# Kernel tuning notes

Hardware: AMD Instinct MI355X
Metric: run time of the kernel (lower is better)

The kernel has to match this reference:

```python
import jax, jax.numpy as jnp
import numpy as np

B, N, E, DIN, DH = 32, 2000, 64000, 128, 128


def setup_inputs() -> dict:
    key = jax.random.key(0)
    ks = jax.random.split(key, 8)
    gene_emb = jax.random.normal(ks[0], (B, N, DIN), dtype=jnp.float32)
    edge_src = jax.random.randint(ks[1], (E,), 0, N, dtype=jnp.int32)
    edge_dst = jax.random.randint(ks[2], (E,), 0, N, dtype=jnp.int32)
    s1 = 1.0 / np.sqrt(DIN)
    s2 = 1.0 / np.sqrt(DH)
    W1 = jax.random.normal(ks[3], (DIN, DH), dtype=jnp.float32) * s1
    b1 = jnp.zeros((DH,), dtype=jnp.float32)
    W2 = jax.random.normal(ks[4], (DH, DH), dtype=jnp.float32) * s2
    b2 = jnp.zeros((DH,), dtype=jnp.float32)
    return {"gene_emb": gene_emb, "edge_src": edge_src, "edge_dst": edge_dst,
            "W1": W1, "b1": b1, "W2": W2, "b2": b2, "pathway_idx": 0}


def _gcn_conv(x, src, dst, norm_e, self_norm, W, b):
    # x: [B, N, Din] -> [B, N, Dout]; PyG GCNConv: linear first, then normalized aggregation
    h = jnp.einsum('bnd,de->bne', x, W)
    msgs = h[:, src, :] * norm_e[None, :, None]          # [B, E, Dout] gather
    agg = jax.vmap(lambda m: jax.ops.segment_sum(m, dst, num_segments=h.shape[1]))(msgs)
    # self-loop contribution (A+I): norm = dinv[i]^2
    return agg + h * self_norm[None, :, None] + b


def reference(gene_emb, edge_src, edge_dst, W1, b1, W2, b2, pathway_idx):
    n = gene_emb.shape[1]
    # symmetric GCN normalization with self loops: deg[i] = in_degree + 1
    deg = jnp.zeros((n,), dtype=gene_emb.dtype).at[edge_dst].add(1.0) + 1.0
    dinv = jax.lax.rsqrt(deg)
    norm_e = dinv[edge_src] * dinv[edge_dst]
    self_norm = dinv * dinv
    x = jax.nn.relu(_gcn_conv(gene_emb, edge_src, edge_dst, norm_e, self_norm, W1, b1))
    x = _gcn_conv(x, edge_src, edge_dst, norm_e, self_norm, W2, b2)
    # global_mean_pool over each graph copy (all graphs have n nodes)
    return jnp.mean(x, axis=1)  # [B, DH]
```

## Files before the change

kernel.cpp:

```cpp
#include <hip/hip_runtime.h>

namespace {
constexpr int NB = 32;
constexpr int NN = 2000;
constexpr int NE = 64000;
constexpr int ND = 128;
constexpr int TR = 32;
constexpr int NCHUNK = (NN + TR - 1) / TR;
constexpr int NXCD = 8;
constexpr int BPB = 2;
constexpr int PAIRS = NB / (NXCD * BPB);
constexpr int GRID_FUSED = NXCD * PAIRS * NCHUNK;
constexpr int SL = 80;
constexpr int ECAP = 1536;

constexpr int CVT_BLOCKS  = 8000;
constexpr int NODE_BLOCKS = 250;
constexpr int W_BLOCKS    = 8;
constexpr int PREP_GRID   = CVT_BLOCKS + NODE_BLOCKS + W_BLOCKS;

constexpr size_t OFF_CNT  = 0;
constexpr size_t OFF_OCNT = 8192;
constexpr size_t OFF_SLI  = 16384;
constexpr size_t OFF_SLO  = OFF_SLI + (size_t)NN * SL * 4;
constexpr size_t OFF_WF   = OFF_SLO + (size_t)NN * SL * 4;
constexpr size_t OFF_XBF  = OFF_WF + 32768;
constexpr size_t OFF_YP   = OFF_XBF + (size_t)NB * NN * ND * 2;

typedef __attribute__((ext_vector_type(8))) short bf16x8;
typedef __attribute__((ext_vector_type(4))) float f32x4;

__device__ __forceinline__ ushort f32_to_bf16(float f) {
    uint u = __float_as_uint(f);
    u += 0x7fffu + ((u >> 16) & 1u);
    return (ushort)(u >> 16);
}
__device__ __forceinline__ uint pack_bf16x2(float lo, float hi) {
    return (uint)f32_to_bf16(lo) | ((uint)f32_to_bf16(hi) << 16);
}
}

__global__ void k_prep(const float* __restrict__ X, ushort* __restrict__ xbf,
                       const float* __restrict__ W1, uint* __restrict__ wf,
                       const int* __restrict__ src, const int* __restrict__ dst,
                       int* __restrict__ cnt, int* __restrict__ ocnt,
                       int* __restrict__ slot_in, int* __restrict__ slot_out) {
    const int blk = blockIdx.x;
    const int tid = threadIdx.x;
    if (blk < CVT_BLOCKS) {
        int i = blk * 256 + tid;
        float4 v = ((const float4*)X)[i];
        ushort4 o;
        o.x = f32_to_bf16(v.x);
        o.y = f32_to_bf16(v.y);
        o.z = f32_to_bf16(v.z);
        o.w = f32_to_bf16(v.w);
        ((ushort4*)xbf)[i] = o;
    } else if (blk < CVT_BLOCKS + NODE_BLOCKS) {
        const int base = (blk - CVT_BLOCKS) * 8;
        __shared__ int lcin[8], lcout[8];
        if (tid < 8) { lcin[tid] = 0; lcout[tid] = 0; }
        __syncthreads();
        const int4* s4p = (const int4*)src;
        const int4* d4p = (const int4*)dst;
        for (int i = tid; i < NE / 4; i += 256) {
            int4 s4 = s4p[i], d4 = d4p[i];
            int ss[4] = {s4.x, s4.y, s4.z, s4.w};
            int dd[4] = {d4.x, d4.y, d4.z, d4.w};
            #pragma unroll
            for (int q = 0; q < 4; q++) {
                int j = dd[q] - base;
                if ((unsigned)j < 8u) {
                    int p = atomicAdd(&lcin[j], 1);
                    if (p < SL) slot_in[(size_t)dd[q] * SL + p] = ss[q];
                }
                int j2 = ss[q] - base;
                if ((unsigned)j2 < 8u) {
                    int p2 = atomicAdd(&lcout[j2], 1);
                    if (p2 < SL) slot_out[(size_t)ss[q] * SL + p2] = dd[q];
                }
            }
        }
        __syncthreads();
        if (tid < 8) {
            cnt[base + tid]  = lcin[tid];
            ocnt[base + tid] = lcout[tid];
        }
    } else {
        int g = (blk - CVT_BLOCKS - NODE_BLOCKS) * 256 + tid;
        int lane = g & 63, f = g >> 6;
        int nt = f >> 2, kc = f & 3;
        int col = nt * 16 + (lane & 15);
        int k0  = kc * 32 + (lane >> 4) * 8;
        uint4 o;
        o.x = pack_bf16x2(W1[(k0 + 0) * ND + col], W1[(k0 + 1) * ND + col]);
        o.y = pack_bf16x2(W1[(k0 + 2) * ND + col], W1[(k0 + 3) * ND + col]);
        o.z = pack_bf16x2(W1[(k0 + 4) * ND + col], W1[(k0 + 5) * ND + col]);
        o.w = pack_bf16x2(W1[(k0 + 6) * ND + col], W1[(k0 + 7) * ND + col]);
        ((uint4*)wf)[g] = o;
    }
}

__global__ __launch_bounds__(256, 4) void k_fused(const ushort* __restrict__ xbf,
                                                  const int* __restrict__ cnt,
                                                  const int* __restrict__ ocnt,
                                                  const int* __restrict__ slot_in,
                                                  const int* __restrict__ slot_out,
                                                  const uint* __restrict__ wfrag,
                                                  const float* __restrict__ b1,
                                                  float* __restrict__ ypart) {
    __shared__ uint  AsU[2][32 * 68];
    __shared__ int2  sEdge[ECAP];
    __shared__ int   sCnt[32];
    __shared__ int   sBase[33];
    __shared__ float sDinv[32];
    __shared__ float sWn[32];
    __shared__ float yred[2][128];
    const int tid = threadIdx.x;

    const int L     = blockIdx.x;
    const int xcd   = L & (NXCD - 1);
    const int sl    = L >> 3;
    const int pair  = sl / NCHUNK;
    const int chunk = sl % NCHUNK;
    const int b0    = xcd * (BPB * PAIRS) + pair * BPB;
    const int n0    = chunk * TR;

    if (tid < 32) {
        int n = n0 + tid;
        int cr = (n < NN) ? cnt[n] : 0;
        sCnt[tid]  = min(cr, SL);
        sDinv[tid] = rsqrtf((float)(cr + 1));
    }
    if (tid < 128) { yred[0][tid] = 0.f; yred[1][tid] = 0.f; }
    __syncthreads();
    if (tid == 0) {
        int s = 0;
        for (int j = 0; j < 32; j++) { sBase[j] = s; s += sCnt[j]; }
        sBase[32] = s;
    }

    const int wv = tid >> 6, ln = tid & 63;

    for (int ii = 0; ii < 8; ii++) {
        const int j = wv * 8 + ii;
        const int n = n0 + j;
        float part = 0.f;
        if (n < NN) {
            int oc = min(ocnt[n], SL);
            const int* op = &slot_out[(size_t)n * SL];
            for (int base = 0; base < oc; base += 64)
                if (base + ln < oc)
                    part += rsqrtf((float)(cnt[op[base + ln]] + 1));
        }
        #pragma unroll
        for (int off = 32; off; off >>= 1) part += __shfl_down(part, off, 64);
        if (ln == 0) {
            float d = sDinv[j];
            sWn[j] = (n < NN) ? d * (d + part) : 0.f;
        }
    }
    __syncthreads();
    const bool staged = (sBase[32] <= ECAP);

    if (staged) {
        for (int ii = 0; ii < 8; ii++) {
            int j = wv * 8 + ii;
            int c = sCnt[j];
            float dd = sDinv[j];
            const int* sp = &slot_in[(size_t)(n0 + j) * SL];
            for (int base = 0; base < c; base += 64) {
                if (base + ln < c) {
                    int sidx = sp[base + ln];
                    float w = rsqrtf((float)(cnt[sidx] + 1)) * dd;
                    sEdge[sBase[j] + base + ln] = make_int2(sidx, __float_as_int(w));
                }
            }
        }
    }
    __syncthreads();

    const uint* __restrict__ Xu0 = (const uint*)(xbf + (size_t)b0 * NN * ND);
    const uint* __restrict__ Xu1 = (const uint*)(xbf + (size_t)(b0 + 1) * NN * ND);
    #pragma unroll 1
    for (int ii = 0; ii < 8; ii++) {
        const int j = wv * 8 + ii;
        const int n = n0 + j;
        float2 a0 = make_float2(0.f, 0.f), a1 = a0, a0b = a0, a1b = a0;
        if (n < NN) {
            float sn = sDinv[j]; sn *= sn;
            uint u0 = Xu0[n * 64 + ln], u1 = Xu1[n * 64 + ln];
            a0.x = sn * __uint_as_float(u0 << 16);
            a0.y = sn * __uint_as_float(u0 & 0xffff0000u);
            a1.x = sn * __uint_as_float(u1 << 16);
            a1.y = sn * __uint_as_float(u1 & 0xffff0000u);
            const int c = sCnt[j];
            if (staged) {
                const int e0 = sBase[j], e1 = e0 + c;
                int e = e0;
                for (; e + 8 <= e1; e += 8) {
                    int sidx[8]; float w[8]; uint q0[8], q1[8];
                    #pragma unroll
                    for (int q = 0; q < 8; q++) {
                        int2 ed = sEdge[e + q];
                        sidx[q] = ed.x; w[q] = __int_as_float(ed.y);
                    }
                    #pragma unroll
                    for (int q = 0; q < 8; q++) {
                        q0[q] = Xu0[sidx[q] * 64 + ln];
                        q1[q] = Xu1[sidx[q] * 64 + ln];
                    }
                    #pragma unroll
                    for (int q = 0; q < 8; q++) {
                        float x0l = __uint_as_float(q0[q] << 16);
                        float x0h = __uint_as_float(q0[q] & 0xffff0000u);
                        float x1l = __uint_as_float(q1[q] << 16);
                        float x1h = __uint_as_float(q1[q] & 0xffff0000u);
                        if (q & 1) {
                            a0b.x = fmaf(w[q], x0l, a0b.x);
                            a0b.y = fmaf(w[q], x0h, a0b.y);
                            a1b.x = fmaf(w[q], x1l, a1b.x);
                            a1b.y = fmaf(w[q], x1h, a1b.y);
                        } else {
                            a0.x = fmaf(w[q], x0l, a0.x);
                            a0.y = fmaf(w[q], x0h, a0.y);
                            a1.x = fmaf(w[q], x1l, a1.x);
                            a1.y = fmaf(w[q], x1h, a1.y);
                        }
                    }
                }
                for (; e < e1; e++) {
                    int2 ed = sEdge[e];
                    float w = __int_as_float(ed.y);
                    uint u0e = Xu0[ed.x * 64 + ln], u1e = Xu1[ed.x * 64 + ln];
                    a0.x = fmaf(w, __uint_as_float(u0e << 16), a0.x);
                    a0.y = fmaf(w, __uint_as_float(u0e & 0xffff0000u), a0.y);
                    a1.x = fmaf(w, __uint_as_float(u1e << 16), a1.x);
                    a1.y = fmaf(w, __uint_as_float(u1e & 0xffff0000u), a1.y);
                }
            } else {
                const int* sp = &slot_in[(size_t)n * SL];
                float dd = sDinv[j];
                for (int e = 0; e < c; e++) {
                    int sidx = sp[e];
                    float w = rsqrtf((float)(cnt[sidx] + 1)) * dd;
                    uint u0e = Xu0[sidx * 64 + ln], u1e = Xu1[sidx * 64 + ln];
                    a0.x = fmaf(w, __uint_as_float(u0e << 16), a0.x);
                    a0.y = fmaf(w, __uint_as_float(u0e & 0xffff0000u), a0.y);
                    a1.x = fmaf(w, __uint_as_float(u1e << 16), a1.x);
                    a1.y = fmaf(w, __uint_as_float(u1e & 0xffff0000u), a1.y);
                }
            }
            a0.x += a0b.x; a0.y += a0b.y;
            a1.x += a1b.x; a1.y += a1b.y;
        }
        AsU[0][j * 68 + ln] = pack_bf16x2(a0.x, a0.y);
        AsU[1][j * 68 + ln] = pack_bf16x2(a1.x, a1.y);
    }
    __syncthreads();

    const int lane15 = ln & 15, quad = ln >> 4;
    f32x4 zero4 = {0.f, 0.f, 0.f, 0.f};
    f32x4 acc[2][2][2];
    #pragma unroll
    for (int b = 0; b < 2; b++)
        #pragma unroll
        for (int mt = 0; mt < 2; mt++)
            #pragma unroll
            for (int nt2 = 0; nt2 < 2; nt2++) acc[b][mt][nt2] = zero4;

    bf16x8 wfr[2][4];
    const bf16x8* Wf8 = (const bf16x8*)wfrag;
    #pragma unroll
    for (int nt2 = 0; nt2 < 2; nt2++)
        #pragma unroll
        for (int kc = 0; kc < 4; kc++)
            wfr[nt2][kc] = Wf8[(((2 * wv + nt2) * 4 + kc) * 64) + ln];

    const bf16x8* A8_0 = (const bf16x8*)AsU[0];
    const bf16x8* A8_1 = (const bf16x8*)AsU[1];
    #pragma unroll
    for (int mt = 0; mt < 2; mt++) {
        const int r = mt * 16 + lane15;
        #pragma unroll
        for (int kc = 0; kc < 4; kc++) {
            bf16x8 af0 = A8_0[r * 17 + kc * 4 + quad];
            bf16x8 af1 = A8_1[r * 17 + kc * 4 + quad];
            #pragma unroll
            for (int nt2 = 0; nt2 < 2; nt2++) {
                acc[0][mt][nt2] = __builtin_amdgcn_mfma_f32_16x16x32_bf16(
                    af0, wfr[nt2][kc], acc[0][mt][nt2], 0, 0, 0);
                acc[1][mt][nt2] = __builtin_amdgcn_mfma_f32_16x16x32_bf16(
                    af1, wfr[nt2][kc], acc[1][mt][nt2], 0, 0, 0);
            }
        }
    }

    #pragma unroll
    for (int nt2 = 0; nt2 < 2; nt2++) {
        int cg = (2 * wv + nt2) * 16 + lane15;
        float bias = b1[cg];
        #pragma unroll
        for (int b = 0; b < 2; b++) {
            float part = 0.f;
            #pragma unroll
            for (int mt = 0; mt < 2; mt++) {
                f32x4 a = acc[b][mt][nt2];
                #pragma unroll
                for (int r = 0; r < 4; r++) {
                    int m = mt * 16 + quad * 4 + r;
                    part = fmaf(sWn[m], fmaxf(a[r] + bias, 0.f), part);
                }
            }
            atomicAdd(&yred[b][cg], part);
        }
    }
    __syncthreads();
    if (tid < 128)
        ypart[((size_t)b0 * NCHUNK + chunk) * ND + tid] = yred[0][tid];
    else
        ypart[((size_t)(b0 + 1) * NCHUNK + chunk) * ND + (tid - 128)] = yred[1][tid - 128];
}

__global__ __launch_bounds__(128) void k_out(const float* __restrict__ ypart,
                                             const float* __restrict__ W2,
                                             const float* __restrict__ b2,
                                             float* __restrict__ out) {
    __shared__ float ys[128];
    const int b = blockIdx.x;
    const int d = threadIdx.x;
    float s = 0.f;
    for (int c = 0; c < NCHUNK; c++)
        s += ypart[((size_t)b * NCHUNK + c) * ND + d];
    ys[d] = s * (1.f / (float)NN);
    __syncthreads();
    float acc = b2[d];
    #pragma unroll 8
    for (int k = 0; k < 128; k++)
        acc = fmaf(ys[k], W2[k * ND + d], acc);
    out[b * ND + d] = acc;
}

extern "C" void kernel_launch(void* const* d_in, const int* in_sizes, int n_in,
                              void* d_out, int out_size, void* d_ws, size_t ws_size,
                              hipStream_t stream) {
    (void)in_sizes; (void)n_in; (void)out_size; (void)ws_size;
    const float* X   = (const float*)d_in[0];
    const int*   src = (const int*)d_in[1];
    const int*   dst = (const int*)d_in[2];
    const float* W1  = (const float*)d_in[3];
    const float* b1  = (const float*)d_in[4];
    const float* W2  = (const float*)d_in[5];
    const float* b2  = (const float*)d_in[6];
    float* out = (float*)d_out;

    char* ws = (char*)d_ws;
    int*    cnt   = (int*)   (ws + OFF_CNT);
    int*    ocnt  = (int*)   (ws + OFF_OCNT);
    int*    sli   = (int*)   (ws + OFF_SLI);
    int*    slo   = (int*)   (ws + OFF_SLO);
    uint*   wfb   = (uint*)  (ws + OFF_WF);
    ushort* xbf   = (ushort*)(ws + OFF_XBF);
    float*  ypart = (float*) (ws + OFF_YP);

    k_prep<<<PREP_GRID, 256, 0, stream>>>(X, xbf, W1, wfb, src, dst,
                                          cnt, ocnt, sli, slo);
    k_fused<<<GRID_FUSED, 256, 0, stream>>>(xbf, cnt, ocnt, sli, slo, wfb, b1, ypart);
    k_out<<<NB, 128, 0, stream>>>(ypart, W2, b2, out);
}
```

Measured before the change: 184.7 us.

## Build edge slot lists with global atomics and drop shared-memory edge staging

The per-node scan blocks, where each of 250 blocks reads all 64000 edges, are replaced by one thread per edge doing global atomicAdd into cnt/ocnt and slot lists, preceded by a memset of the counters. In the fused kernel the shared-memory sEdge staging pass and its prefix sum are removed. The gather loop now reads slot_in and recomputes the rsqrt edge weights directly, and runs before the out-degree weight loop. This cuts the redundant edge scans and a block barrier, but adds global atomic contention, an extra memset launch, and nondeterministic edge ordering in the float sums.

```diff
diff --git a/kernel.cpp b/kernel.cpp
--- a/kernel.cpp
+++ b/kernel.cpp
@@ -12,12 +12,11 @@
 constexpr int PAIRS = NB / (NXCD * BPB);
 constexpr int GRID_FUSED = NXCD * PAIRS * NCHUNK;
 constexpr int SL = 80;
-constexpr int ECAP = 1536;
 
 constexpr int CVT_BLOCKS  = 8000;
-constexpr int NODE_BLOCKS = 250;
 constexpr int W_BLOCKS    = 8;
-constexpr int PREP_GRID   = CVT_BLOCKS + NODE_BLOCKS + W_BLOCKS;
+constexpr int EDGE_BLOCKS = 250;
+constexpr int FILL_GRID   = CVT_BLOCKS + W_BLOCKS + EDGE_BLOCKS;
 
 constexpr size_t OFF_CNT  = 0;
 constexpr size_t OFF_OCNT = 8192;
@@ -26,6 +25,7 @@
 constexpr size_t OFF_WF   = OFF_SLO + (size_t)NN * SL * 4;
 constexpr size_t OFF_XBF  = OFF_WF + 32768;
 constexpr size_t OFF_YP   = OFF_XBF + (size_t)NB * NN * ND * 2;
+constexpr size_t MEMSET_BYTES = 16384;
 
 typedef __attribute__((ext_vector_type(8))) short bf16x8;
 typedef __attribute__((ext_vector_type(4))) float f32x4;
@@ -40,7 +40,7 @@
 }
 }
 
-__global__ void k_prep(const float* __restrict__ X, ushort* __restrict__ xbf,
+__global__ void k_fill(const float* __restrict__ X, ushort* __restrict__ xbf,
                        const float* __restrict__ W1, uint* __restrict__ wf,
                        const int* __restrict__ src, const int* __restrict__ dst,
                        int* __restrict__ cnt, int* __restrict__ ocnt,
@@ -56,38 +56,8 @@
         o.z = f32_to_bf16(v.z);
         o.w = f32_to_bf16(v.w);
         ((ushort4*)xbf)[i] = o;
-    } else if (blk < CVT_BLOCKS + NODE_BLOCKS) {
-        const int base = (blk - CVT_BLOCKS) * 8;
-        __shared__ int lcin[8], lcout[8];
-        if (tid < 8) { lcin[tid] = 0; lcout[tid] = 0; }
-        __syncthreads();
-        const int4* s4p = (const int4*)src;
-        const int4* d4p = (const int4*)dst;
-        for (int i = tid; i < NE / 4; i += 256) {
-            int4 s4 = s4p[i], d4 = d4p[i];
-            int ss[4] = {s4.x, s4.y, s4.z, s4.w};
-            int dd[4] = {d4.x, d4.y, d4.z, d4.w};
-            #pragma unroll
-            for (int q = 0; q < 4; q++) {
-                int j = dd[q] - base;
-                if ((unsigned)j < 8u) {
-                    int p = atomicAdd(&lcin[j], 1);
-                    if (p < SL) slot_in[(size_t)dd[q] * SL + p] = ss[q];
-                }
-                int j2 = ss[q] - base;
-                if ((unsigned)j2 < 8u) {
-                    int p2 = atomicAdd(&lcout[j2], 1);
-                    if (p2 < SL) slot_out[(size_t)ss[q] * SL + p2] = dd[q];
-                }
-            }
-        }
-        __syncthreads();
-        if (tid < 8) {
-            cnt[base + tid]  = lcin[tid];
-            ocnt[base + tid] = lcout[tid];
-        }
-    } else {
-        int g = (blk - CVT_BLOCKS - NODE_BLOCKS) * 256 + tid;
+    } else if (blk < CVT_BLOCKS + W_BLOCKS) {
+        int g = (blk - CVT_BLOCKS) * 256 + tid;
         int lane = g & 63, f = g >> 6;
         int nt = f >> 2, kc = f & 3;
         int col = nt * 16 + (lane & 15);
@@ -98,6 +68,13 @@
         o.z = pack_bf16x2(W1[(k0 + 4) * ND + col], W1[(k0 + 5) * ND + col]);
         o.w = pack_bf16x2(W1[(k0 + 6) * ND + col], W1[(k0 + 7) * ND + col]);
         ((uint4*)wf)[g] = o;
+    } else {
+        int e = (blk - CVT_BLOCKS - W_BLOCKS) * 256 + tid;
+        int s = src[e], d = dst[e];
+        int p = atomicAdd(&cnt[d], 1);
+        if (p < SL) slot_in[(size_t)d * SL + p] = s;
+        int q = atomicAdd(&ocnt[s], 1);
+        if (q < SL) slot_out[(size_t)s * SL + q] = d;
     }
 }
 
@@ -110,9 +87,7 @@
                                                   const float* __restrict__ b1,
                                                   float* __restrict__ ypart) {
     __shared__ uint  AsU[2][32 * 68];
-    __shared__ int2  sEdge[ECAP];
     __shared__ int   sCnt[32];
-    __shared__ int   sBase[33];
     __shared__ float sDinv[32];
     __shared__ float sWn[32];
     __shared__ float yred[2][128];
@@ -134,13 +109,73 @@
     }
     if (tid < 128) { yred[0][tid] = 0.f; yred[1][tid] = 0.f; }
     __syncthreads();
-    if (tid == 0) {
-        int s = 0;
-        for (int j = 0; j < 32; j++) { sBase[j] = s; s += sCnt[j]; }
-        sBase[32] = s;
-    }
 
     const int wv = tid >> 6, ln = tid & 63;
+
+    const uint* __restrict__ Xu0 = (const uint*)(xbf + (size_t)b0 * NN * ND);
+    const uint* __restrict__ Xu1 = (const uint*)(xbf + (size_t)(b0 + 1) * NN * ND);
+    #pragma unroll 1
+    for (int ii = 0; ii < 8; ii++) {
+        const int j = wv * 8 + ii;
+        const int n = n0 + j;
+        float2 a0 = make_float2(0.f, 0.f), a1 = a0, a0b = a0, a1b = a0;
+        if (n < NN) {
+            const float dd = sDinv[j];
+            float sn = dd * dd;
+            uint u0 = Xu0[n * 64 + ln], u1 = Xu1[n * 64 + ln];
+            a0.x = sn * __uint_as_float(u0 << 16);
+            a0.y = sn * __uint_as_float(u0 & 0xffff0000u);
+            a1.x = sn * __uint_as_float(u1 << 16);
+            a1.y = sn * __uint_as_float(u1 & 0xffff0000u);
+            const int c = sCnt[j];
+            const int* sp = &slot_in[(size_t)n * SL];
+            int e = 0;
+            for (; e + 8 <= c; e += 8) {
+                int sidx[8]; float w[8]; uint q0[8], q1[8];
+                #pragma unroll
+                for (int q = 0; q < 8; q++) sidx[q] = sp[e + q];
+                #pragma unroll
+                for (int q = 0; q < 8; q++) {
+                    q0[q] = Xu0[sidx[q] * 64 + ln];
+                    q1[q] = Xu1[sidx[q] * 64 + ln];
+                }
+                #pragma unroll
+                for (int q = 0; q < 8; q++)
+                    w[q] = rsqrtf((float)(cnt[sidx[q]] + 1)) * dd;
+                #pragma unroll
+                for (int q = 0; q < 8; q++) {
+                    float x0l = __uint_as_float(q0[q] << 16);
+                    float x0h = __uint_as_float(q0[q] & 0xffff0000u);
+                    float x1l = __uint_as_float(q1[q] << 16);
+                    float x1h = __uint_as_float(q1[q] & 0xffff0000u);
+                    if (q & 1) {
+                        a0b.x = fmaf(w[q], x0l, a0b.x);
+                        a0b.y = fmaf(w[q], x0h, a0b.y);
+                        a1b.x = fmaf(w[q], x1l, a1b.x);
+                        a1b.y = fmaf(w[q], x1h, a1b.y);
+                    } else {
+                        a0.x = fmaf(w[q], x0l, a0.x);
+                        a0.y = fmaf(w[q], x0h, a0.y);
+                        a1.x = fmaf(w[q], x1l, a1.x);
+                        a1.y = fmaf(w[q], x1h, a1.y);
+                    }
+                }
+            }
+            for (; e < c; e++) {
+                int sidx = sp[e];
+                float w = rsqrtf((float)(cnt[sidx] + 1)) * dd;
+                uint u0e = Xu0[sidx * 64 + ln], u1e = Xu1[sidx * 64 + ln];
+                a0.x = fmaf(w, __uint_as_float(u0e << 16), a0.x);
+                a0.y = fmaf(w, __uint_as_float(u0e & 0xffff0000u), a0.y);
+                a1.x = fmaf(w, __uint_as_float(u1e << 16), a1.x);
+                a1.y = fmaf(w, __uint_as_float(u1e & 0xffff0000u), a1.y);
+            }
+            a0.x += a0b.x; a0.y += a0b.y;
+            a1.x += a1b.x; a1.y += a1b.y;
+        }
+        AsU[0][j * 68 + ln] = pack_bf16x2(a0.x, a0.y);
+        AsU[1][j * 68 + ln] = pack_bf16x2(a1.x, a1.y);
+    }
 
     for (int ii = 0; ii < 8; ii++) {
         const int j = wv * 8 + ii;
@@ -159,103 +194,6 @@
             float d = sDinv[j];
             sWn[j] = (n < NN) ? d * (d + part) : 0.f;
         }
-    }
-    __syncthreads();
-    const bool staged = (sBase[32] <= ECAP);
-
-    if (staged) {
-        for (int ii = 0; ii < 8; ii++) {
-            int j = wv * 8 + ii;
-            int c = sCnt[j];
-            float dd = sDinv[j];
-            const int* sp = &slot_in[(size_t)(n0 + j) * SL];
-            for (int base = 0; base < c; base += 64) {
-                if (base + ln < c) {
-                    int sidx = sp[base + ln];
-                    float w = rsqrtf((float)(cnt[sidx] + 1)) * dd;
-                    sEdge[sBase[j] + base + ln] = make_int2(sidx, __float_as_int(w));
-                }
-            }
-        }
-    }
-    __syncthreads();
-
-    const uint* __restrict__ Xu0 = (const uint*)(xbf + (size_t)b0 * NN * ND);
-    const uint* __restrict__ Xu1 = (const uint*)(xbf + (size_t)(b0 + 1) * NN * ND);
-    #pragma unroll 1
-    for (int ii = 0; ii < 8; ii++) {
-        const int j = wv * 8 + ii;
-        const int n = n0 + j;
-        float2 a0 = make_float2(0.f, 0.f), a1 = a0, a0b = a0, a1b = a0;
-        if (n < NN) {
-            float sn = sDinv[j]; sn *= sn;
-            uint u0 = Xu0[n * 64 + ln], u1 = Xu1[n * 64 + ln];
-            a0.x = sn * __uint_as_float(u0 << 16);
-            a0.y = sn * __uint_as_float(u0 & 0xffff0000u);
-            a1.x = sn * __uint_as_float(u1 << 16);
-            a1.y = sn * __uint_as_float(u1 & 0xffff0000u);
-            const int c = sCnt[j];
-            if (staged) {
-                const int e0 = sBase[j], e1 = e0 + c;
-                int e = e0;
-                for (; e + 8 <= e1; e += 8) {
-                    int sidx[8]; float w[8]; uint q0[8], q1[8];
-                    #pragma unroll
-                    for (int q = 0; q < 8; q++) {
-                        int2 ed = sEdge[e + q];
-                        sidx[q] = ed.x; w[q] = __int_as_float(ed.y);
-                    }
-                    #pragma unroll
-                    for (int q = 0; q < 8; q++) {
-                        q0[q] = Xu0[sidx[q] * 64 + ln];
-                        q1[q] = Xu1[sidx[q] * 64 + ln];
-                    }
-                    #pragma unroll
-                    for (int q = 0; q < 8; q++) {
-                        float x0l = __uint_as_float(q0[q] << 16);
-                        float x0h = __uint_as_float(q0[q] & 0xffff0000u);
-                        float x1l = __uint_as_float(q1[q] << 16);
-                        float x1h = __uint_as_float(q1[q] & 0xffff0000u);
-                        if (q & 1) {
-                            a0b.x = fmaf(w[q], x0l, a0b.x);
-                            a0b.y = fmaf(w[q], x0h, a0b.y);
-                            a1b.x = fmaf(w[q], x1l, a1b.x);
-                            a1b.y = fmaf(w[q], x1h, a1b.y);
-                        } else {
-                            a0.x = fmaf(w[q], x0l, a0.x);
-                            a0.y = fmaf(w[q], x0h, a0.y);
-                            a1.x = fmaf(w[q], x1l, a1.x);
-                            a1.y = fmaf(w[q], x1h, a1.y);
-                        }
-                    }
-                }
-                for (; e < e1; e++) {
-                    int2 ed = sEdge[e];
-                    float w = __int_as_float(ed.y);
-                    uint u0e = Xu0[ed.x * 64 + ln], u1e = Xu1[ed.x * 64 + ln];
-                    a0.x = fmaf(w, __uint_as_float(u0e << 16), a0.x);
-                    a0.y = fmaf(w, __uint_as_float(u0e & 0xffff0000u), a0.y);
-                    a1.x = fmaf(w, __uint_as_float(u1e << 16), a1.x);
-                    a1.y = fmaf(w, __uint_as_float(u1e & 0xffff0000u), a1.y);
-                }
-            } else {
-                const int* sp = &slot_in[(size_t)n * SL];
-                float dd = sDinv[j];
-                for (int e = 0; e < c; e++) {
-                    int sidx = sp[e];
-                    float w = rsqrtf((float)(cnt[sidx] + 1)) * dd;
-                    uint u0e = Xu0[sidx * 64 + ln], u1e = Xu1[sidx * 64 + ln];
-                    a0.x = fmaf(w, __uint_as_float(u0e << 16), a0.x);
-                    a0.y = fmaf(w, __uint_as_float(u0e & 0xffff0000u), a0.y);
-                    a1.x = fmaf(w, __uint_as_float(u1e << 16), a1.x);
-                    a1.y = fmaf(w, __uint_as_float(u1e & 0xffff0000u), a1.y);
-                }
-            }
-            a0.x += a0b.x; a0.y += a0b.y;
-            a1.x += a1b.x; a1.y += a1b.y;
-        }
-        AsU[0][j * 68 + ln] = pack_bf16x2(a0.x, a0.y);
-        AsU[1][j * 68 + ln] = pack_bf16x2(a1.x, a1.y);
     }
     __syncthreads();
 
@@ -363,7 +301,8 @@
     ushort* xbf   = (ushort*)(ws + OFF_XBF);
     float*  ypart = (float*) (ws + OFF_YP);
 
-    k_prep<<<PREP_GRID, 256, 0, stream>>>(X, xbf, W1, wfb, src, dst,
+    (void)hipMemsetAsync(ws, 0, MEMSET_BYTES, stream);
+    k_fill<<<FILL_GRID, 256, 0, stream>>>(X, xbf, W1, wfb, src, dst,
                                           cnt, ocnt, sli, slo);
     k_fused<<<GRID_FUSED, 256, 0, stream>>>(xbf, cnt, ocnt, sli, slo, wfb, b1, ypart);
     k_out<<<NB, 128, 0, stream>>>(ypart, W2, b2, out);
```

Result: faster. 179.4 us (-2.9%).
